# Optimization experiments

Measured on AMD Instinct MI355X. Metric: run time of the kernel, lower is better.

## Reference

```python
import jax, jax.numpy as jnp
import numpy as np

B, C, IMG, P = 32, 3, 224, 16
E, NH, M, L = 768, 12, 3072, 12
D = E // NH          # head_dim = 64
N = (IMG // P) ** 2 + 1  # 197 tokens incl. class token


def setup_inputs() -> dict:
    key = jax.random.key(0)
    ks = jax.random.split(key, 8)
    r = lambda k, s: jax.random.normal(k, s, jnp.float32) * 0.02
    return {
        "x": jax.random.normal(ks[0], (B, C, IMG, IMG), jnp.float32),
        "conv_w": r(ks[1], (E, C, P, P)),
        "conv_b": jnp.zeros((E,), jnp.float32),
        "cls_tok": jnp.zeros((1, 1, E), jnp.float32),
        "pos_enc": r(ks[2], (1, N, E)),
        "qkv_w": r(ks[3], (L, E, 3 * E)),
        "qkv_b": jnp.zeros((L, 3 * E), jnp.float32),
        "qn_g": jnp.ones((L, D), jnp.float32), "qn_b": jnp.zeros((L, D), jnp.float32),
        "kn_g": jnp.ones((L, D), jnp.float32), "kn_b": jnp.zeros((L, D), jnp.float32),
        "proj_w": r(ks[4], (L, E, E)), "proj_b": jnp.zeros((L, E), jnp.float32),
        "ln1_g": jnp.ones((L, E), jnp.float32), "ln1_b": jnp.zeros((L, E), jnp.float32),
        "w1": r(ks[5], (L, E, M)), "b1": jnp.zeros((L, M), jnp.float32),
        "w2": r(ks[6], (L, M, E)), "b2": jnp.zeros((L, E), jnp.float32),
        "ln2_g": jnp.ones((L, E), jnp.float32), "ln2_b": jnp.zeros((L, E), jnp.float32),
    }


def _ln(x, g, b, eps=1e-5):
    m = x.mean(-1, keepdims=True)
    v = ((x - m) ** 2).mean(-1, keepdims=True)
    return (x - m) * jax.lax.rsqrt(v + eps) * g + b


def _forward(x, conv_w, conv_b, cls_tok, pos_enc, params):
    bs = x.shape[0]
    hp = x.shape[2] // P
    # stride-P conv patch embedding == patchify + linear
    patches = x.reshape(bs, C, hp, P, hp, P).transpose(0, 2, 4, 1, 3, 5).reshape(bs, hp * hp, C * P * P)
    h = patches @ conv_w.reshape(E, C * P * P).T + conv_b  # [B, n_patches, E]
    h = jnp.concatenate([jnp.broadcast_to(cls_tok, (bs, 1, E)), h], axis=1) + pos_enc

    def block(h, pr):
        (qw, qb, qg, qbb, kg, kbb, pw, pb, l1g, l1b, W1, B1, W2, B2, l2g, l2b) = pr
        res = h
        qkv = (h @ qw + qb).reshape(bs, N, 3, NH, D).transpose(2, 0, 3, 1, 4)  # [3,B,H,N,D]
        q, k, v = qkv[0], qkv[1], qkv[2]
        q = _ln(q, qg, qbb)
        k = _ln(k, kg, kbb)
        attn = jax.nn.softmax(jnp.einsum('bhnd,bhmd->bhnm', q, k) / jnp.sqrt(jnp.float32(D)), axis=-1)
        o = jnp.einsum('bhnm,bhmd->bhnd', attn, v).transpose(0, 2, 1, 3).reshape(bs, N, E)
        o = o @ pw + pb
        h = _ln(o, l1g, l1b) + res          # post-attn: LN(attn_out) + residual (as in source)
        res2 = h
        f = jax.nn.gelu(h @ W1 + B1, approximate=False) @ W2 + B2
        h = _ln(f, l2g, l2b) + res2
        return h, None

    h, _ = jax.lax.scan(block, h, params)
    return h[:, 0, :]


def reference(x, conv_w, conv_b, cls_tok, pos_enc, qkv_w, qkv_b, qn_g, qn_b, kn_g, kn_b,
              proj_w, proj_b, ln1_g, ln1_b, w1, b1, w2, b2, ln2_g, ln2_b):
    params = (qkv_w, qkv_b, qn_g, qn_b, kn_g, kn_b, proj_w, proj_b,
              ln1_g, ln1_b, w1, b1, w2, b2, ln2_g, ln2_b)
    return _forward(x, conv_w, conv_b, cls_tok, pos_enc, params)
```

## Files before the change

### kernel.cpp

```cpp
#include <hip/hip_runtime.h>

#define B_    32
#define NTOK  197
#define E_    768
#define NH_   12
#define M_    3072
#define L_    12
#define NPAT  196
#define BN    (B_*NTOK)
#define BNP   (B_*NPAT)

typedef unsigned short bf16_t;
typedef short v8s __attribute__((ext_vector_type(8)));
typedef float v4f __attribute__((ext_vector_type(4)));
typedef unsigned short u16x8 __attribute__((ext_vector_type(8)));

__device__ inline float bf2f(bf16_t u){
    union { unsigned int i; float f; } c; c.i = ((unsigned int)u) << 16; return c.f;
}
__device__ inline bf16_t f2bf(float f){
    union { float f; unsigned int i; } c; c.f = f;
    unsigned int u = c.i;
    u += 0x7FFFu + ((u >> 16) & 1u);
    return (bf16_t)(u >> 16);
}
__device__ inline float lo16f(unsigned int u){
    union { unsigned int i; float f; } c; c.i = u << 16; return c.f;
}
__device__ inline float hi16f(unsigned int u){
    union { unsigned int i; float f; } c; c.i = u & 0xFFFF0000u; return c.f;
}
__device__ inline float wave_rsum(float x){
    #pragma unroll
    for (int off = 32; off; off >>= 1) x += __shfl_xor(x, off);
    return x;
}
__device__ inline float wave_rmax(float x){
    #pragma unroll
    for (int off = 32; off; off >>= 1) x = fmaxf(x, __shfl_xor(x, off));
    return x;
}

__global__ __launch_bounds__(256) void detect_k(const unsigned short* __restrict__ x,
                                                int n, int* __restrict__ flag){
    int cnt = 0;
    for (int i = blockIdx.x*256 + threadIdx.x; i < n; i += 256*64)
        { unsigned short u = x[i]; if (((u >> 7) & 0xFFu) == 0xFFu) ++cnt; }
    if (cnt) atomicAdd(flag, cnt);
}

__global__ __launch_bounds__(256) void convert_k(const void* __restrict__ src,
    bf16_t* __restrict__ dst, int n, const int* __restrict__ flag){
    int i = blockIdx.x*256 + threadIdx.x;
    if (i >= n) return;
    if (*flag >= 8) dst[i] = f2bf(((const float*)src)[i]);
    else            dst[i] = ((const bf16_t*)src)[i];
}

__global__ __launch_bounds__(256) void convert_t_k(const void* __restrict__ src,
    bf16_t* __restrict__ dst, int K, int N, const int* __restrict__ flag){
    __shared__ float tile[32][33];
    const int l  = blockIdx.z;
    const int n0 = blockIdx.x*32, k0 = blockIdx.y*32;
    const int c  = threadIdx.x & 31, r = threadIdx.x >> 5;
    const bool isf = (*flag >= 8);
    const size_t ibase = (size_t)l*(size_t)K*N;
    #pragma unroll
    for (int i = 0; i < 4; ++i){
        int kk = k0 + r + i*8;
        float v;
        if (isf) v = ((const float*)src)[ibase + (size_t)kk*N + n0 + c];
        else     v = bf2f(((const bf16_t*)src)[ibase + (size_t)kk*N + n0 + c]);
        tile[r + i*8][c] = v;
    }
    __syncthreads();
    #pragma unroll
    for (int i = 0; i < 4; ++i){
        int nn = n0 + r + i*8;
        dst[ibase + (size_t)nn*K + k0 + c] = f2bf(tile[c][r + i*8]);
    }
}

template<int AT, int BT, int OT, int ACT>
__global__ __launch_bounds__(256) void gemm_ab(
    const void* __restrict__ A, const bf16_t* __restrict__ Bw,
    const bf16_t* __restrict__ bias, void* __restrict__ C,
    int Mr, int Nc, int K)
{
    __shared__ float As[16][72];
    __shared__ float Bs[16][72];
    const int tx = threadIdx.x, ty = threadIdx.y;
    const int t  = ty*16 + tx;
    const int m0 = blockIdx.y*64, n0 = blockIdx.x*64;
    float acc[4][4] = {};

    for (int k0 = 0; k0 < K; k0 += 16){
        {
            int mm = t >> 2, kk = (t & 3)*4;
            int row = m0 + mm;
            float f0=0.f,f1=0.f,f2=0.f,f3=0.f;
            if (row < Mr){
                if (AT == 0){
                    const float4 v4 = *(const float4*)((const float*)A + (size_t)row*K + k0 + kk);
                    f0=v4.x; f1=v4.y; f2=v4.z; f3=v4.w;
                } else {
                    const ushort4 u4 = *(const ushort4*)((const bf16_t*)A + (size_t)row*K + k0 + kk);
                    f0=bf2f(u4.x); f1=bf2f(u4.y); f2=bf2f(u4.z); f3=bf2f(u4.w);
                }
            }
            As[kk+0][mm]=f0; As[kk+1][mm]=f1; As[kk+2][mm]=f2; As[kk+3][mm]=f3;
        }
        if (BT){
            int nn = t >> 2, kk = (t & 3)*4;
            const ushort4 u4 = *(const ushort4*)(Bw + (size_t)(n0+nn)*K + k0 + kk);
            Bs[kk+0][nn]=bf2f(u4.x); Bs[kk+1][nn]=bf2f(u4.y);
            Bs[kk+2][nn]=bf2f(u4.z); Bs[kk+3][nn]=bf2f(u4.w);
        } else {
            int kk = t >> 4, nn = (t & 15)*4;
            const ushort4 u4 = *(const ushort4*)(Bw + (size_t)(k0+kk)*Nc + n0 + nn);
            Bs[kk][nn+0]=bf2f(u4.x); Bs[kk][nn+1]=bf2f(u4.y);
            Bs[kk][nn+2]=bf2f(u4.z); Bs[kk][nn+3]=bf2f(u4.w);
        }
        __syncthreads();
        #pragma unroll
        for (int kk = 0; kk < 16; ++kk){
            float4 av = *(const float4*)&As[kk][ty*4];
            float4 bv = *(const float4*)&Bs[kk][tx*4];
            float a_[4] = {av.x, av.y, av.z, av.w};
            float b_[4] = {bv.x, bv.y, bv.z, bv.w};
            #pragma unroll
            for (int i=0;i<4;i++)
                #pragma unroll
                for (int j=0;j<4;j++)
                    acc[i][j] += a_[i]*b_[j];
        }
        __syncthreads();
    }
    #pragma unroll
    for (int i=0;i<4;i++){
        int m = m0 + ty*4 + i;
        if (m >= Mr) continue;
        #pragma unroll
        for (int j=0;j<4;j++){
            int n = n0 + tx*4 + j;
            float v = acc[i][j];
            if (bias) v += bf2f(bias[n]);
            if (ACT==1) v = 0.5f*v*(1.f + erff(v*0.70710678118654752f));
            if (OT == 0) ((float*)C)[(size_t)m*Nc + n] = v;
            else         ((bf16_t*)C)[(size_t)m*Nc + n] = f2bf(v);
        }
    }
}

template<int OT, int ACT>
__global__ __launch_bounds__(256) void gemm_mfma(
    const bf16_t* __restrict__ A, const bf16_t* __restrict__ Bt,
    const bf16_t* __restrict__ bias, void* __restrict__ C,
    int Mr, int Nc, int K)
{
    __shared__ __align__(16) char As[128*32*2];
    __shared__ __align__(16) char Bs[128*32*2];
    const int t    = threadIdx.x;
    const int lane = t & 63;
    const int wave = t >> 6;
    const int wr = wave >> 1, wc = wave & 1;
    const int m0 = blockIdx.y * 128, n0 = blockIdx.x * 128;

    const int srow = t >> 1, shalf = t & 1;
    int arow = m0 + srow; if (arow >= Mr) arow = Mr - 1;
    const bf16_t* ag = A  + (size_t)arow * K + shalf * 16;
    const bf16_t* bg = Bt + (size_t)(n0 + srow) * K + shalf * 16;
    const int wbase = srow*64 + shalf*32;
    const int wswz  = (srow & 7) << 4;
    const int w0 = (wbase)      ^ wswz;
    const int w1 = (wbase + 16) ^ wswz;

    const int fr = lane & 15, fg = lane >> 4;
    int aoff[4], boff[4];
    #pragma unroll
    for (int s = 0; s < 4; ++s){
        int ar = wr*64 + s*16 + fr;
        int br = wc*64 + s*16 + fr;
        aoff[s] = (ar*64 + fg*16) ^ ((ar & 7) << 4);
        boff[s] = (br*64 + fg*16) ^ ((br & 7) << 4);
    }

    const v4f vzero = {0.f, 0.f, 0.f, 0.f};
    v4f acc[4][4];
    #pragma unroll
    for (int i = 0; i < 4; ++i)
        #pragma unroll
        for (int j = 0; j < 4; ++j)
            acc[i][j] = vzero;

    for (int k0 = 0; k0 < K; k0 += 32){
        u16x8 a0 = *(const u16x8*)(ag + k0);
        u16x8 a1 = *(const u16x8*)(ag + k0 + 8);
        u16x8 b0 = *(const u16x8*)(bg + k0);
        u16x8 b1 = *(const u16x8*)(bg + k0 + 8);
        __syncthreads();
        *(u16x8*)(As + w0) = a0;
        *(u16x8*)(As + w1) = a1;
        *(u16x8*)(Bs + w0) = b0;
        *(u16x8*)(Bs + w1) = b1;
        __syncthreads();
        v8s af[4], bfv[4];
        #pragma unroll
        for (int s = 0; s < 4; ++s){
            af[s]  = *(const v8s*)(As + aoff[s]);
            bfv[s] = *(const v8s*)(Bs + boff[s]);
        }
        #pragma unroll
        for (int i = 0; i < 4; ++i)
            #pragma unroll
            for (int j = 0; j < 4; ++j)
                acc[i][j] = __builtin_amdgcn_mfma_f32_16x16x32_bf16(af[i], bfv[j], acc[i][j], 0, 0, 0);
    }

    #pragma unroll
    for (int i = 0; i < 4; ++i){
        #pragma unroll
        for (int r = 0; r < 4; ++r){
            int m = m0 + wr*64 + i*16 + fg*4 + r;
            if (m >= Mr) continue;
            #pragma unroll
            for (int j = 0; j < 4; ++j){
                int n = n0 + wc*64 + j*16 + fr;
                float v = acc[i][j][r];
                if (bias) v += bf2f(bias[n]);
                if (ACT == 1) v = 0.5f*v*(1.f + erff(v*0.70710678118654752f));
                if (OT == 0) ((float*)C)[(size_t)m*Nc + n] = v;
                else         ((bf16_t*)C)[(size_t)m*Nc + n] = f2bf(v);
            }
        }
    }
}

__global__ __launch_bounds__(256) void patchify_k(const bf16_t* __restrict__ x, float* __restrict__ out){
    int idx = blockIdx.x*256 + threadIdx.x;
    if (idx >= BNP*E_) return;
    int kk  = idx % 768;
    int bnp = idx / 768;
    int b = bnp / 196, np = bnp % 196;
    int ph = np / 14,  pw = np % 14;
    int c = kk >> 8, rr = kk & 255;
    int i = rr >> 4, j = rr & 15;
    size_t xi = (((size_t)(b*3 + c))*224 + (ph*16 + i))*224 + (pw*16 + j);
    out[idx] = bf2f(x[xi]);
}

__global__ __launch_bounds__(256) void patchify_bf_k(const bf16_t* __restrict__ x, bf16_t* __restrict__ out){
    int idx = blockIdx.x*256 + threadIdx.x;
    if (idx >= BNP*E_) return;
    int kk  = idx % 768;
    int bnp = idx / 768;
    int b = bnp / 196, np = bnp % 196;
    int ph = np / 14,  pw = np % 14;
    int c = kk >> 8, rr = kk & 255;
    int i = rr >> 4, j = rr & 15;
    size_t xi = (((size_t)(b*3 + c))*224 + (ph*16 + i))*224 + (pw*16 + j);
    out[idx] = x[xi];
}

__global__ __launch_bounds__(256) void assemble_k(const float* __restrict__ pe,
    const bf16_t* __restrict__ cls, const bf16_t* __restrict__ pos,
    float* __restrict__ h, bf16_t* __restrict__ hb){
    int idx = blockIdx.x*256 + threadIdx.x;
    if (idx >= BN*E_) return;
    int e = idx % 768; int bn = idx / 768;
    int b = bn / 197,  n  = bn % 197;
    float v = (n == 0) ? bf2f(cls[e]) : pe[((size_t)b*196 + (n-1))*768 + e];
    float r = v + bf2f(pos[n*768 + e]);
    h[idx]  = r;
    hb[idx] = f2bf(r);
}

__global__ __launch_bounds__(256) void qkv_split_ln_k(const bf16_t* __restrict__ qkv,
    const bf16_t* __restrict__ qg, const bf16_t* __restrict__ qb,
    const bf16_t* __restrict__ kg, const bf16_t* __restrict__ kb,
    bf16_t* __restrict__ q, bf16_t* __restrict__ k, bf16_t* __restrict__ v){
    int lane = threadIdx.x & 63;
    int item = blockIdx.x*4 + (threadIdx.x >> 6);
    if (item >= BN*NH_) return;
    int bn = item / NH_, h = item % NH_;
    int b = bn / 197,   n = bn % 197;
    size_t src = (size_t)bn*2304 + h*64 + lane;
    size_t dst = (((size_t)(b*NH_ + h))*197 + n)*64 + lane;
    {
        float xv = bf2f(qkv[src]);
        float mu  = wave_rsum(xv) * (1.f/64.f);
        float dd  = xv - mu;
        float var = wave_rsum(dd*dd) * (1.f/64.f);
        q[dst] = f2bf((dd * rsqrtf(var + 1e-5f) * bf2f(qg[lane]) + bf2f(qb[lane])) * 0.125f);
    }
    {
        float xv = bf2f(qkv[src + 768]);
        float mu  = wave_rsum(xv) * (1.f/64.f);
        float dd  = xv - mu;
        float var = wave_rsum(dd*dd) * (1.f/64.f);
        k[dst] = f2bf(dd * rsqrtf(var + 1e-5f) * bf2f(kg[lane]) + bf2f(kb[lane]));
    }
    v[dst] = qkv[src + 1536];
}

__global__ __launch_bounds__(256) void vtrans_k(const bf16_t* __restrict__ vn, bf16_t* __restrict__ vt){
    __shared__ bf16_t tl[32][34];
    const int bh = blockIdx.z;
    const int m0 = blockIdx.x*32, d0 = blockIdx.y*32;
    const int c = threadIdx.x & 31, r = threadIdx.x >> 5;
    const bf16_t* src = vn + (size_t)bh*197*64;
    #pragma unroll
    for (int k = 0; k < 4; ++k){
        int m = m0 + r + 8*k;
        tl[r + 8*k][c] = (m < 197) ? src[(size_t)m*64 + d0 + c] : (bf16_t)0;
    }
    __syncthreads();
    bf16_t* dst = vt + (size_t)bh*64*224;
    #pragma unroll
    for (int k = 0; k < 4; ++k){
        int d = d0 + r + 8*k;
        dst[(size_t)d*224 + m0 + c] = tl[c][r + 8*k];
    }
}

#define PST 232
__global__ __launch_bounds__(64) void attn_mfma_k(const bf16_t* __restrict__ qn,
    const bf16_t* __restrict__ kn, const bf16_t* __restrict__ vt, bf16_t* __restrict__ o){
    __shared__ __align__(16) bf16_t P[16*PST];
    const int lane = threadIdx.x;
    const int i = lane & 15, g = lane >> 4;
    const int bh = blockIdx.y;
    const int b = bh / NH_, h = bh % NH_;
    const int q0 = blockIdx.x * 16;
    const bf16_t* qb = qn + (size_t)bh*197*64;
    const bf16_t* kb = kn + (size_t)bh*197*64;
    const bf16_t* vb = vt + (size_t)bh*64*224;

    {
        int r = lane >> 2, c0 = 208 + (lane & 3)*4;
        ushort4 z = {0,0,0,0};
        *(ushort4*)&P[r*PST + c0] = z;
    }

    int qrow = q0 + i; if (qrow > 196) qrow = 196;
    const v8s qa0 = *(const v8s*)(qb + (size_t)qrow*64 + 8*g);
    const v8s qa1 = *(const v8s*)(qb + (size_t)qrow*64 + 32 + 8*g);

    v4f s[13];
    #pragma unroll
    for (int t = 0; t < 13; ++t) s[t] = (v4f){0.f,0.f,0.f,0.f};
    #pragma unroll
    for (int t = 0; t < 13; ++t){
        int m = 16*t + i; if (m > 196) m = 196;
        const bf16_t* kr = kb + (size_t)m*64;
        v8s kf0 = *(const v8s*)(kr + 8*g);
        v8s kf1 = *(const v8s*)(kr + 32 + 8*g);
        s[t] = __builtin_amdgcn_mfma_f32_16x16x32_bf16(qa0, kf0, s[t], 0, 0, 0);
        s[t] = __builtin_amdgcn_mfma_f32_16x16x32_bf16(qa1, kf1, s[t], 0, 0, 0);
    }

    float mx[4], sum[4];
    #pragma unroll
    for (int r = 0; r < 4; ++r){
        float m_ = -1e30f;
        #pragma unroll
        for (int t = 0; t < 13; ++t){
            float v = s[t][r];
            if (16*t + i > 196) v = -1e30f;
            m_ = fmaxf(m_, v);
        }
        #pragma unroll
        for (int off = 1; off < 16; off <<= 1) m_ = fmaxf(m_, __shfl_xor(m_, off));
        mx[r] = m_;
        sum[r] = 0.f;
    }
    #pragma unroll
    for (int t = 0; t < 13; ++t){
        #pragma unroll
        for (int r = 0; r < 4; ++r){
            float v = (16*t + i > 196) ? 0.f : __expf(s[t][r] - mx[r]);
            sum[r] += v;
            P[(4*g + r)*PST + 16*t + i] = f2bf(v);
        }
    }
    #pragma unroll
    for (int r = 0; r < 4; ++r){
        float s_ = sum[r];
        #pragma unroll
        for (int off = 1; off < 16; off <<= 1) s_ += __shfl_xor(s_, off);
        sum[r] = 1.f / s_;
    }

    v4f oacc[4];
    #pragma unroll
    for (int j = 0; j < 4; ++j) oacc[j] = (v4f){0.f,0.f,0.f,0.f};
    #pragma unroll
    for (int kc = 0; kc < 7; ++kc){
        v8s pa = *(const v8s*)&P[i*PST + kc*32 + 8*g];
        #pragma unroll
        for (int j = 0; j < 4; ++j){
            v8s vf = *(const v8s*)(vb + (size_t)(16*j + i)*224 + kc*32 + 8*g);
            oacc[j] = __builtin_amdgcn_mfma_f32_16x16x32_bf16(pa, vf, oacc[j], 0, 0, 0);
        }
    }

    #pragma unroll
    for (int r = 0; r < 4; ++r){
        int n = q0 + 4*g + r;
        if (n < 197){
            bf16_t* op = o + ((size_t)(b*197 + n))*768 + h*64;
            #pragma unroll
            for (int j = 0; j < 4; ++j)
                op[16*j + i] = f2bf(oacc[j][r] * sum[r]);
        }
    }
}

__global__ __launch_bounds__(256) void attn_blk_k(const bf16_t* __restrict__ qn,
    const bf16_t* __restrict__ kn, const bf16_t* __restrict__ vn, bf16_t* __restrict__ o){
    __shared__ unsigned int ktp[32][203];
    __shared__ unsigned int vtp[64][105];
    __shared__ float qly[4][64];
    __shared__ float ply[4][256];
    const int lane = threadIdx.x & 63, wave = threadIdx.x >> 6;
    const int bh = blockIdx.y;
    const int b = bh / NH_, h = bh % NH_;
    const bf16_t* kb = kn + (size_t)bh*197*64;
    const bf16_t* vb = vn + (size_t)bh*197*64;

    for (int m = wave; m < 210; m += 4){
        bf16_t kv = 0, vv = 0;
        if (m < 197){ kv = kb[(size_t)m*64 + lane]; vv = vb[(size_t)m*64 + lane]; }
        if (m < 203)
            ((bf16_t*)ktp)[((size_t)(lane >> 1)*203 + m)*2 + (lane & 1)] = kv;
        ((bf16_t*)vtp)[((size_t)lane*105 + (m >> 1))*2 + (m & 1)] = vv;
    }
    __syncthreads();

    const int n0 = blockIdx.x*16 + wave*4;
    for (int i = 0; i < 4; ++i){
        int n = n0 + i;
        int nn = (n < 197) ? n : 196;
        qly[wave][lane] = bf2f(qn[((size_t)bh*197 + nn)*64 + lane]);
        float s0 = 0.f, s1 = 0.f, s2 = 0.f, s3 = 0.f;
        const int m3 = (lane < 5) ? lane + 192 : 196;
        #pragma unroll 8
        for (int d2 = 0; d2 < 32; ++d2){
            float2 q2 = *(const float2*)&qly[wave][2*d2];
            unsigned int k0 = ktp[d2][lane];
            unsigned int k1 = ktp[d2][lane + 64];
            unsigned int k2 = ktp[d2][lane + 128];
            unsigned int k3 = ktp[d2][m3];
            s0 += q2.x * lo16f(k0) + q2.y * hi16f(k0);
            s1 += q2.x * lo16f(k1) + q2.y * hi16f(k1);
            s2 += q2.x * lo16f(k2) + q2.y * hi16f(k2);
            s3 += q2.x * lo16f(k3) + q2.y * hi16f(k3);
        }
        if (lane >= 5) s3 = -1e30f;
        float mx = wave_rmax(fmaxf(fmaxf(s0, s1), fmaxf(s2, s3)));
        float p0 = expf(s0 - mx), p1 = expf(s1 - mx), p2 = expf(s2 - mx);
        float p3 = (lane < 5) ? expf(s3 - mx) : 0.f;
        float sum = wave_rsum(p0 + p1 + p2 + p3);
        float inv = 1.f / sum;
        ply[wave][lane      ] = p0*inv;
        ply[wave][lane +  64] = p1*inv;
        ply[wave][lane + 128] = p2*inv;
        ply[wave][lane + 192] = p3*inv;
        float acc = 0.f;
        #pragma unroll 4
        for (int m2 = 0; m2 < 99; ++m2){
            float2 p2v = *(const float2*)&ply[wave][2*m2];
            unsigned int vv = vtp[lane][m2];
            acc += p2v.x * lo16f(vv) + p2v.y * hi16f(vv);
        }
        if (n < 197) o[((size_t)(b*197 + n))*768 + h*64 + lane] = f2bf(acc);
    }
}

__global__ __launch_bounds__(256) void lnadd_k(const float* __restrict__ src,
    const bf16_t* __restrict__ g, const bf16_t* __restrict__ b,
    float* __restrict__ h, bf16_t* __restrict__ hb){
    __shared__ float red[256];
    int t = threadIdx.x;
    size_t row = blockIdx.x;
    const float* p = src + row*768;
    float x0 = p[t], x1 = p[t+256], x2 = p[t+512];
    red[t] = x0 + x1 + x2;
    __syncthreads();
    for (int off = 128; off; off >>= 1){ if (t < off) red[t] += red[t+off]; __syncthreads(); }
    float mean = red[0] * (1.f/768.f);
    __syncthreads();
    float d0 = x0-mean, d1 = x1-mean, d2 = x2-mean;
    red[t] = d0*d0 + d1*d1 + d2*d2;
    __syncthreads();
    for (int off = 128; off; off >>= 1){ if (t < off) red[t] += red[t+off]; __syncthreads(); }
    float inv = rsqrtf(red[0]*(1.f/768.f) + 1e-5f);
    float* hp = h + row*768;
    bf16_t* hq = hb + row*768;
    float r0 = hp[t]     + d0*inv*bf2f(g[t])     + bf2f(b[t]);
    float r1 = hp[t+256] + d1*inv*bf2f(g[t+256]) + bf2f(b[t+256]);
    float r2 = hp[t+512] + d2*inv*bf2f(g[t+512]) + bf2f(b[t+512]);
    hp[t] = r0;     hq[t] = f2bf(r0);
    hp[t+256] = r1; hq[t+256] = f2bf(r1);
    hp[t+512] = r2; hq[t+512] = f2bf(r2);
}

__global__ __launch_bounds__(256) void outcopy_k(const float* __restrict__ h, float* __restrict__ out){
    int idx = blockIdx.x*256 + threadIdx.x;
    if (idx >= B_*E_) return;
    int b = idx / 768, e = idx % 768;
    out[idx] = h[(size_t)b*197*768 + e];
}

#define OFF_T1   ((size_t)19365888)
#define OFF_R    ((size_t)38731776)
#define OFF_QN   ((size_t)(38731776 + 29048832))
#define OFF_KN   ((size_t)(67780608 + 9682944))
#define OFF_VN   ((size_t)(77463552 + 9682944))
#define OFF_FLAG ((size_t)96829440)
#define OFF_CONV ((size_t)96829696)

extern "C" void kernel_launch(void* const* d_in, const int* in_sizes, int n_in,
                              void* d_out, int out_size, void* d_ws, size_t ws_size,
                              hipStream_t stream) {
    (void)out_size;
    char* wsb = (char*)d_ws;
    float*  h       = (float*)(wsb);
    float*  t1      = (float*)(wsb + OFF_T1);
    bf16_t* abf     = (bf16_t*)(wsb + OFF_T1);
    bf16_t* qkvbuf  = (bf16_t*)(wsb + OFF_R);
    bf16_t* patches = (bf16_t*)(wsb + OFF_R);
    float*  patchf  = (float*)(wsb + OFF_R);
    float*  projout = (float*)(wsb + OFF_R);
    bf16_t* fbuf    = (bf16_t*)(wsb + OFF_R);
    bf16_t* vtb     = (bf16_t*)(wsb + OFF_R);
    bf16_t* qnb     = (bf16_t*)(wsb + OFF_QN);
    bf16_t* knb     = (bf16_t*)(wsb + OFF_KN);
    bf16_t* vnb     = (bf16_t*)(wsb + OFF_VN);
    bf16_t* habf    = (bf16_t*)(wsb + OFF_VN);
    int*    flag    = (int*)(wsb + OFF_FLAG);

    size_t conv_total = 0;
    for (int i = 0; i < n_in; ++i) conv_total += (((size_t)in_sizes[i]*2) + 15) & ~(size_t)15;
    const bool hedge = (ws_size >= OFF_CONV + conv_total);

    const bf16_t* inp[21];
    if (hedge){
        hipMemsetAsync(flag, 0, 4, stream);
        detect_k<<<64, 256, 0, stream>>>((const unsigned short*)d_in[0], in_sizes[0], flag);
        size_t off = 0;
        for (int i = 0; i < n_in && i < 21; ++i){
            bf16_t* dst = (bf16_t*)(wsb + OFF_CONV + off);
            if (i == 5)
                convert_t_k<<<dim3(2304/32, 768/32, 12), 256, 0, stream>>>(d_in[i], dst, 768, 2304, flag);
            else if (i == 11)
                convert_t_k<<<dim3(768/32, 768/32, 12), 256, 0, stream>>>(d_in[i], dst, 768, 768, flag);
            else if (i == 15)
                convert_t_k<<<dim3(3072/32, 768/32, 12), 256, 0, stream>>>(d_in[i], dst, 768, 3072, flag);
            else if (i == 17)
                convert_t_k<<<dim3(768/32, 3072/32, 12), 256, 0, stream>>>(d_in[i], dst, 3072, 768, flag);
            else
                convert_k<<<(in_sizes[i] + 255)/256, 256, 0, stream>>>(d_in[i], dst, in_sizes[i], flag);
            inp[i] = dst;
            off += (((size_t)in_sizes[i]*2) + 15) & ~(size_t)15;
        }
    } else {
        for (int i = 0; i < n_in && i < 21; ++i) inp[i] = (const bf16_t*)d_in[i];
    }

    if (hedge){
        patchify_bf_k<<<(BNP*E_ + 255)/256, 256, 0, stream>>>(inp[0], patches);
        gemm_mfma<0,0><<<dim3(E_/128, BNP/128), 256, 0, stream>>>(
            patches, inp[1], inp[2], t1, BNP, E_, 768);
        assemble_k<<<(BN*E_ + 255)/256, 256, 0, stream>>>(t1, inp[3], inp[4], h, habf);

        for (int l = 0; l < L_; ++l){
            gemm_mfma<1,0><<<dim3(2304/128, (BN+127)/128), 256, 0, stream>>>(
                habf, inp[5] + (size_t)l*E_*2304, inp[6] + (size_t)l*2304, qkvbuf, BN, 2304, 768);
            qkv_split_ln_k<<<(BN*NH_)/4, 256, 0, stream>>>(
                qkvbuf, inp[7] + l*64, inp[8] + l*64, inp[9] + l*64, inp[10] + l*64,
                qnb, knb, vnb);
            vtrans_k<<<dim3(7, 2, B_*NH_), 256, 0, stream>>>(vnb, vtb);
            attn_mfma_k<<<dim3(13, B_*NH_), 64, 0, stream>>>(qnb, knb, vtb, abf);
            gemm_mfma<0,0><<<dim3(E_/128, (BN+127)/128), 256, 0, stream>>>(
                abf, inp[11] + (size_t)l*E_*E_, inp[12] + (size_t)l*E_, projout, BN, E_, 768);
            lnadd_k<<<BN, 256, 0, stream>>>(projout, inp[13] + l*E_, inp[14] + l*E_, h, habf);
            gemm_mfma<1,1><<<dim3(M_/128, (BN+127)/128), 256, 0, stream>>>(
                habf, inp[15] + (size_t)l*E_*M_, inp[16] + (size_t)l*M_, fbuf, BN, M_, 768);
            gemm_mfma<0,0><<<dim3(E_/128, (BN+127)/128), 256, 0, stream>>>(
                fbuf, inp[17] + (size_t)l*M_*E_, inp[18] + (size_t)l*E_, t1, BN, E_, 3072);
            lnadd_k<<<BN, 256, 0, stream>>>(t1, inp[19] + l*E_, inp[20] + l*E_, h, habf);
        }
    } else {
        dim3 gblk(16, 16);
        patchify_k<<<(BNP*E_ + 255)/256, 256, 0, stream>>>(inp[0], patchf);
        gemm_ab<0,1,0,0><<<dim3(E_/64, BNP/64), gblk, 0, stream>>>(
            patchf, inp[1], inp[2], t1, BNP, E_, 768);
        assemble_k<<<(BN*E_ + 255)/256, 256, 0, stream>>>(t1, inp[3], inp[4], h, habf);
        for (int l = 0; l < L_; ++l){
            gemm_ab<0,0,1,0><<<dim3(2304/64, (BN+63)/64), gblk, 0, stream>>>(
                h, inp[5] + (size_t)l*E_*2304, inp[6] + (size_t)l*2304, qkvbuf, BN, 2304, E_);
            qkv_split_ln_k<<<(BN*NH_)/4, 256, 0, stream>>>(
                qkvbuf, inp[7] + l*64, inp[8] + l*64, inp[9] + l*64, inp[10] + l*64,
                qnb, knb, vnb);
            attn_blk_k<<<dim3(13, B_*NH_), 256, 0, stream>>>(qnb, knb, vnb, abf);
            gemm_ab<1,0,0,0><<<dim3(E_/64, (BN+63)/64), gblk, 0, stream>>>(
                abf, inp[11] + (size_t)l*E_*E_, inp[12] + (size_t)l*E_, projout, BN, E_, E_);
            lnadd_k<<<BN, 256, 0, stream>>>(projout, inp[13] + l*E_, inp[14] + l*E_, h, habf);
            gemm_ab<0,0,1,1><<<dim3(M_/64, (BN+63)/64), gblk, 0, stream>>>(
                h, inp[15] + (size_t)l*E_*M_, inp[16] + (size_t)l*M_, fbuf, BN, M_, E_);
            gemm_ab<1,0,0,0><<<dim3(E_/64, (BN+63)/64), gblk, 0, stream>>>(
                fbuf, inp[17] + (size_t)l*M_*E_, inp[18] + (size_t)l*E_, t1, BN, E_, M_);
            lnadd_k<<<BN, 256, 0, stream>>>(t1, inp[19] + l*E_, inp[20] + l*E_, h, habf);
        }
    }

    outcopy_k<<<(B_*E_ + 255)/256, 256, 0, stream>>>(h, (float*)d_out);
}
```

Before: 5.178 ms.

## Load GEMM tiles directly global-to-LDS with BK=64 and XOR swizzle

The MFMA GEMM now uses global_load_lds so tiles go straight from global memory into LDS without passing through registers. The K step doubles from 32 to 64, with a new per-wave row mapping and XOR-swizzled chunk layout to avoid bank conflicts. This halves the number of barriers per K and removes register staging, at the cost of twice the LDS per block. There is still no double buffering, so loads remain exposed, and K must be a multiple of 64.

```diff
diff --git a/kernel.cpp b/kernel.cpp
--- a/kernel.cpp
+++ b/kernel.cpp
@@ -39,6 +39,11 @@
     #pragma unroll
     for (int off = 32; off; off >>= 1) x = fmaxf(x, __shfl_xor(x, off));
     return x;
+}
+__device__ inline void gl2l16(const void* g, void* l){
+    typedef __attribute__((address_space(1))) void gv_t;
+    typedef __attribute__((address_space(3))) void lv_t;
+    __builtin_amdgcn_global_load_lds((gv_t*)(size_t)g, (lv_t*)l, 16, 0, 0);
 }
 
 __global__ __launch_bounds__(256) void detect_k(const unsigned short* __restrict__ x,
@@ -158,31 +163,37 @@
     const bf16_t* __restrict__ bias, void* __restrict__ C,
     int Mr, int Nc, int K)
 {
-    __shared__ __align__(16) char As[128*32*2];
-    __shared__ __align__(16) char Bs[128*32*2];
+    __shared__ __align__(16) char As[128*128];
+    __shared__ __align__(16) char Bs[128*128];
     const int t    = threadIdx.x;
     const int lane = t & 63;
     const int wave = t >> 6;
     const int wr = wave >> 1, wc = wave & 1;
     const int m0 = blockIdx.y * 128, n0 = blockIdx.x * 128;
 
-    const int srow = t >> 1, shalf = t & 1;
-    int arow = m0 + srow; if (arow >= Mr) arow = Mr - 1;
-    const bf16_t* ag = A  + (size_t)arow * K + shalf * 16;
-    const bf16_t* bg = Bt + (size_t)(n0 + srow) * K + shalf * 16;
-    const int wbase = srow*64 + shalf*32;
-    const int wswz  = (srow & 7) << 4;
-    const int w0 = (wbase)      ^ wswz;
-    const int w1 = (wbase + 16) ^ wswz;
+    const int sub  = lane >> 3;
+    const int kch  = (lane & 7) ^ sub;
+    const bf16_t* aB[4];
+    const bf16_t* bB[4];
+    #pragma unroll
+    for (int i = 0; i < 4; ++i){
+        int ar = m0 + wave*32 + i*8 + sub;
+        if (ar >= Mr) ar = Mr - 1;
+        aB[i] = A  + (size_t)ar * K + kch*8;
+        bB[i] = Bt + (size_t)(n0 + wave*32 + i*8 + sub) * K + kch*8;
+    }
+    char* aL = As + wave*4096;
+    char* bL = Bs + wave*4096;
 
     const int fr = lane & 15, fg = lane >> 4;
-    int aoff[4], boff[4];
-    #pragma unroll
-    for (int s = 0; s < 4; ++s){
-        int ar = wr*64 + s*16 + fr;
-        int br = wc*64 + s*16 + fr;
-        aoff[s] = (ar*64 + fg*16) ^ ((ar & 7) << 4);
-        boff[s] = (br*64 + fg*16) ^ ((br & 7) << 4);
+    const int key = (fr & 7) << 4;
+    const int kf0 = (fg*16)      ^ key;
+    const int kf1 = (64 + fg*16) ^ key;
+    int arb[4], brb[4];
+    #pragma unroll
+    for (int fi = 0; fi < 4; ++fi){
+        arb[fi] = (wr*64 + fi*16 + fr) * 128;
+        brb[fi] = (wc*64 + fi*16 + fr) * 128;
     }
 
     const v4f vzero = {0.f, 0.f, 0.f, 0.f};
@@ -193,28 +204,29 @@
         for (int j = 0; j < 4; ++j)
             acc[i][j] = vzero;
 
-    for (int k0 = 0; k0 < K; k0 += 32){
-        u16x8 a0 = *(const u16x8*)(ag + k0);
-        u16x8 a1 = *(const u16x8*)(ag + k0 + 8);
-        u16x8 b0 = *(const u16x8*)(bg + k0);
-        u16x8 b1 = *(const u16x8*)(bg + k0 + 8);
+    for (int k0 = 0; k0 < K; k0 += 64){
+        #pragma unroll
+        for (int i = 0; i < 4; ++i){
+            gl2l16(aB[i] + k0, aL + i*1024);
+            gl2l16(bB[i] + k0, bL + i*1024);
+        }
         __syncthreads();
-        *(u16x8*)(As + w0) = a0;
-        *(u16x8*)(As + w1) = a1;
-        *(u16x8*)(Bs + w0) = b0;
-        *(u16x8*)(Bs + w1) = b1;
+        #pragma unroll
+        for (int s = 0; s < 2; ++s){
+            const int kf = s ? kf1 : kf0;
+            v8s af[4], bfv[4];
+            #pragma unroll
+            for (int fi = 0; fi < 4; ++fi){
+                af[fi]  = *(const v8s*)(As + arb[fi] + kf);
+                bfv[fi] = *(const v8s*)(Bs + brb[fi] + kf);
+            }
+            #pragma unroll
+            for (int i = 0; i < 4; ++i)
+                #pragma unroll
+                for (int j = 0; j < 4; ++j)
+                    acc[i][j] = __builtin_amdgcn_mfma_f32_16x16x32_bf16(af[i], bfv[j], acc[i][j], 0, 0, 0);
+        }
         __syncthreads();
-        v8s af[4], bfv[4];
-        #pragma unroll
-        for (int s = 0; s < 4; ++s){
-            af[s]  = *(const v8s*)(As + aoff[s]);
-            bfv[s] = *(const v8s*)(Bs + boff[s]);
-        }
-        #pragma unroll
-        for (int i = 0; i < 4; ++i)
-            #pragma unroll
-            for (int j = 0; j < 4; ++j)
-                acc[i][j] = __builtin_amdgcn_mfma_f32_16x16x32_bf16(af[i], bfv[j], acc[i][j], 0, 0, 0);
     }
 
     #pragma unroll
```

After: 4.894 ms. 5.5% less time.
